# Kernel tuning notes

Measured on AMD Instinct MI355X. Metric: run time of the kernel, lower is better.

The kernel has to match this reference:

```python
import jax, jax.numpy as jnp
import numpy as np

B = 64                      # batch_size
MAX_STEPS = 100
FEAT = 6 + MAX_STEPS        # 106
REPEATS = 10
D = REPEATS * FEAT          # 1060
H = 256                     # policy_hidden_size
COUNTS = 32 * np.arange(B) + 16   # ragged segment sizes, sum=65536, max=2032
N = int(COUNTS.sum())
MAXLEN = int(COUNTS.max())
BN_EPS = 1e-5
LRELU_SLOPE = 0.01


def setup_inputs() -> dict:
    key = jax.random.key(0)
    k = jax.random.split(key, 6)
    seg = np.repeat(np.arange(B), COUNTS).astype(np.float32)  # column 0 = batch index
    features = jax.random.normal(k[0], (N, 1 + FEAT), jnp.float32)
    features = features.at[:, 0].set(jnp.asarray(seg))
    W1 = jax.random.normal(k[1], (D, H), jnp.float32) / np.sqrt(D)
    b1 = jax.random.normal(k[2], (H,), jnp.float32) * 0.01
    W2 = jax.random.normal(k[3], (H, 1), jnp.float32) / np.sqrt(H)
    b2 = jax.random.normal(k[4], (1,), jnp.float32) * 0.01
    return {
        "features": features,
        "bn_gamma": jnp.ones((D,), jnp.float32),
        "bn_beta": jnp.zeros((D,), jnp.float32),
        "W1": W1, "b1": b1, "W2": W2, "b2": b2,
        "max_len": MAXLEN,
    }


def reference(features, bn_gamma, bn_beta, W1, b1, W2, b2, max_len):
    seg = features[:, 0].astype(jnp.int32)                 # [N] batch indices
    x = jnp.tile(features[:, 1:], (1, REPEATS))            # [N, D] repeated features
    # BatchNorm1d (training mode: biased batch stats, as in the torch default)
    mean = jnp.mean(x, axis=0)
    var = jnp.var(x, axis=0)
    xn = (x - mean) * jax.lax.rsqrt(var + BN_EPS) * bn_gamma + bn_beta
    h = jnp.dot(xn, W1) + b1                               # [N, H]
    h = jnp.where(h >= 0, h, LRELU_SLOPE * h)              # LeakyReLU
    logits = (jnp.dot(h, W2) + b2)[:, 0]                   # [N]
    # segmented (ragged) log_softmax over each batch element's nodes
    m = jax.ops.segment_max(logits, seg, num_segments=B)   # [B]
    z = logits - m[seg]
    s = jax.ops.segment_sum(jnp.exp(z), seg, num_segments=B)
    logp = z - jnp.log(s)[seg]                             # [N]
    # scatter into padded [B, max_len] (-inf padding), position = rank within segment
    cnts = jax.ops.segment_sum(jnp.ones_like(seg), seg, num_segments=B)
    starts = jnp.cumsum(cnts) - cnts                       # exclusive prefix sum
    pos = jnp.arange(N, dtype=jnp.int32) - starts[seg]
    out = jnp.full((B, max_len), -jnp.inf, jnp.float32)
    return out.at[seg, pos].set(logp)
```

## Files before the change

kernel.cpp:

```cpp
#include <hip/hip_runtime.h>
#include <math.h>

#define NROWS   65536
#define NFEAT   106
#define NCOLIN  107
#define DREP    10
#define HID     256
#define BATCH   64
#define MAXLEN  2032
#define BN_EPS  1e-5f
#define SLOPE   0.01f
#define KPAD    128
#define NB_STATS 512
#define NEG_BIG (-1.0e30f)

#define WS_PART   0
#define WS_BACC   (WS_PART + NB_STATS*212)
#define WS_W1T    (WS_BACC + HID)
#define WS_FT     (WS_W1T + (HID*KPAD)/2)
#define WS_LOGITS (WS_FT + (NROWS*KPAD)/2)

typedef __attribute__((ext_vector_type(8))) short short8v;
typedef __attribute__((ext_vector_type(4))) float f32x4;

__device__ inline unsigned short f2bf(float x) {
    unsigned int u = __float_as_uint(x);
    return (unsigned short)((u + 0x7FFFu + ((u >> 16) & 1u)) >> 16);
}

__device__ __forceinline__ void gload_lds16(const void* g, void* l) {
    __builtin_amdgcn_global_load_lds(
        (const __attribute__((address_space(1))) void*)(g),
        (__attribute__((address_space(3))) void*)(l), 16, 0, 0);
}

__global__ __launch_bounds__(256) void k_stats(const float* __restrict__ feat,
                                               const float* __restrict__ b1,
                                               float* __restrict__ ws) {
    int tid  = threadIdx.x;
    int wave = tid >> 6, lane = tid & 63;
    int gw   = blockIdx.x * 4 + wave;
    if (blockIdx.x == 0) ws[WS_BACC + tid] = b1[tid];

    unsigned char* ft = (unsigned char*)(ws + WS_FT);
    int c0 = 2 * lane, c1 = 2 * lane + 1;
    bool act = (lane < 53);
    float s0 = 0.f, q0 = 0.f, s1 = 0.f, q1 = 0.f;
    for (int r = gw; r < NROWS; r += 2048) {
        const float* row = feat + (size_t)r * NCOLIN + 1;
        float v0 = 0.f, v1 = 0.f;
        if (act) { v0 = row[c0]; v1 = row[c1]; }
        s0 += v0; q0 += v0 * v0;
        s1 += v1; q1 += v1 * v1;
        unsigned int u = ((unsigned int)f2bf(v1) << 16) | f2bf(v0);
        size_t off = (size_t)(r >> 6) * 16384 + (size_t)((r & 63) * 256 + ((lane * 4) ^ ((r & 7) << 4)));
        *(unsigned int*)(ft + off) = u;
    }
    __shared__ float red[4][64][4];
    red[wave][lane][0] = s0; red[wave][lane][1] = q0;
    red[wave][lane][2] = s1; red[wave][lane][3] = q1;
    __syncthreads();
    if (tid < 53) {
        float S0 = 0.f, Q0 = 0.f, S1 = 0.f, Q1 = 0.f;
        for (int w = 0; w < 4; ++w) {
            S0 += red[w][tid][0]; Q0 += red[w][tid][1];
            S1 += red[w][tid][2]; Q1 += red[w][tid][3];
        }
        float* p = ws + WS_PART + blockIdx.x * 212;
        p[2 * tid] = S0; p[2 * tid + 1] = S1;
        p[106 + 2 * tid] = Q0; p[107 + 2 * tid] = Q1;
    }
}

__global__ __launch_bounds__(256) void k_fold2(const float* __restrict__ gamma,
                                               const float* __restrict__ beta,
                                               const float* __restrict__ W1,
                                               float* __restrict__ ws) {
    int k = blockIdx.x;
    int j = threadIdx.x;
    unsigned char* w1t = (unsigned char*)(ws + WS_W1T);
    int byteW = j * 256 + ((2 * k) ^ ((j & 7) << 4));
    if (k >= NFEAT) { *(unsigned short*)(w1t + byteW) = 0; return; }

    float S = ws[WS_PART + j * 212 + k]       + ws[WS_PART + (j + 256) * 212 + k];
    float Q = ws[WS_PART + j * 212 + 106 + k] + ws[WS_PART + (j + 256) * 212 + 106 + k];
    #pragma unroll
    for (int o = 32; o > 0; o >>= 1) { S += __shfl_xor(S, o); Q += __shfl_xor(Q, o); }
    __shared__ float r8[8];
    int w = j >> 6, l = j & 63;
    if (l == 0) { r8[w * 2] = S; r8[w * 2 + 1] = Q; }
    __syncthreads();
    S = r8[0] + r8[2] + r8[4] + r8[6];
    Q = r8[1] + r8[3] + r8[5] + r8[7];

    float mean = S * (1.0f / NROWS);
    float var  = Q * (1.0f / NROWS) - mean * mean;
    float rstd = rsqrtf(var + BN_EPS);

    float accW = 0.f, accB = 0.f;
    #pragma unroll
    for (int r = 0; r < DREP; ++r) {
        int d = r * NFEAT + k;
        float wv = W1[(size_t)d * HID + j];
        accW += gamma[d] * wv;
        accB += beta[d]  * wv;
    }
    float a = accW * rstd;
    *(unsigned short*)(w1t + byteW) = f2bf(a);
    atomicAdd(&ws[WS_BACC + j], accB - mean * a);
}

__global__ __launch_bounds__(256) void k_mlp2(const float* __restrict__ W2,
                                              const float* __restrict__ b2,
                                              float* __restrict__ ws) {
    __shared__ __align__(16) unsigned char lds[81920];
    unsigned char* wl = lds;
    unsigned char* fl = lds + 65536;

    int tid = threadIdx.x;
    int w = tid >> 6, l = tid & 63;
    int lq = l >> 4, ln = l & 15;

    const unsigned char* wsrc = (const unsigned char*)(ws + WS_W1T);
    #pragma unroll
    for (int i = 0; i < 16; ++i)
        gload_lds16(wsrc + (w * 16 + i) * 1024 + l * 16, wl + (w * 16 + i) * 1024);

    float b1r[16], w2r[16];
    #pragma unroll
    for (int ct = 0; ct < 16; ++ct) {
        b1r[ct] = ws[WS_BACC + ct * 16 + ln];
        w2r[ct] = W2[ct * 16 + ln];
    }
    float bias2 = b2[0];
    __syncthreads();

    const unsigned char* ftb = (const unsigned char*)(ws + WS_FT);
    for (int tile = blockIdx.x; tile < NROWS / 64; tile += gridDim.x) {
        const unsigned char* src = ftb + (size_t)tile * 16384 + w * 4096;
        #pragma unroll
        for (int i = 0; i < 4; ++i)
            gload_lds16(src + i * 1024 + l * 16, fl + w * 4096 + i * 1024);
        asm volatile("s_waitcnt vmcnt(0)" ::: "memory");

        int arow = w * 16 + ln;
        short8v a[4];
        #pragma unroll
        for (int ks = 0; ks < 4; ++ks) {
            int kb = ks * 64 + lq * 16;
            a[ks] = *(const short8v*)(fl + arow * 256 + (kb ^ ((arow & 7) << 4)));
        }
        float sp[4] = {0.f, 0.f, 0.f, 0.f};
        #pragma unroll 4
        for (int ct = 0; ct < 16; ++ct) {
            int j = ct * 16 + ln;
            f32x4 acc = {0.f, 0.f, 0.f, 0.f};
            #pragma unroll
            for (int ks = 0; ks < 4; ++ks) {
                int kb = ks * 64 + lq * 16;
                short8v bfg = *(const short8v*)(wl + j * 256 + (kb ^ ((j & 7) << 4)));
                acc = __builtin_amdgcn_mfma_f32_16x16x32_bf16(a[ks], bfg, acc, 0, 0, 0);
            }
            #pragma unroll
            for (int reg = 0; reg < 4; ++reg) {
                float h = acc[reg] + b1r[ct];
                h = (h >= 0.f) ? h : SLOPE * h;
                sp[reg] += h * w2r[ct];
            }
        }
        #pragma unroll
        for (int reg = 0; reg < 4; ++reg) {
            float s = sp[reg];
            s += __shfl_xor(s, 1); s += __shfl_xor(s, 2);
            s += __shfl_xor(s, 4); s += __shfl_xor(s, 8);
            if (ln == 0)
                ws[WS_LOGITS + tile * 64 + w * 16 + lq * 4 + reg] = s + bias2;
        }
    }
}

__global__ __launch_bounds__(256) void k_softmax(const float* __restrict__ ws,
                                                 float* __restrict__ out) {
    int b = blockIdx.x;
    int tid = threadIdx.x;
    int cnt = 32 * b + 16;
    int start = 16 * b * b;
    __shared__ float cache[MAXLEN];
    __shared__ float red[8];
    const float* lg = ws + WS_LOGITS + start;
    for (int i = tid; i < cnt; i += 256) cache[i] = lg[i];
    __syncthreads();

    float m = -1.0e30f;
    for (int i = tid; i < cnt; i += 256) m = fmaxf(m, cache[i]);
    #pragma unroll
    for (int o = 32; o > 0; o >>= 1) m = fmaxf(m, __shfl_xor(m, o));
    int wave = tid >> 6, lane = tid & 63;
    if (lane == 0) red[wave] = m;
    __syncthreads();
    m = fmaxf(fmaxf(red[0], red[1]), fmaxf(red[2], red[3]));

    float s = 0.f;
    for (int i = tid; i < cnt; i += 256) s += expf(cache[i] - m);
    #pragma unroll
    for (int o = 32; o > 0; o >>= 1) s += __shfl_xor(s, o);
    if (lane == 0) red[4 + wave] = s;
    __syncthreads();
    s = red[4] + red[5] + red[6] + red[7];
    float logC = m + logf(s);

    float* op = out + (size_t)b * MAXLEN;
    for (int i = tid; i < MAXLEN; i += 256)
        op[i] = (i < cnt) ? cache[i] - logC : NEG_BIG;
}

extern "C" void kernel_launch(void* const* d_in, const int* in_sizes, int n_in,
                              void* d_out, int out_size, void* d_ws, size_t ws_size,
                              hipStream_t stream) {
    const float* feat  = (const float*)d_in[0];
    const float* gamma = (const float*)d_in[1];
    const float* beta  = (const float*)d_in[2];
    const float* W1    = (const float*)d_in[3];
    const float* b1    = (const float*)d_in[4];
    const float* W2    = (const float*)d_in[5];
    const float* b2    = (const float*)d_in[6];
    float* ws  = (float*)d_ws;
    float* out = (float*)d_out;

    hipLaunchKernelGGL(k_stats,   dim3(NB_STATS), dim3(256), 0, stream, feat, b1, ws);
    hipLaunchKernelGGL(k_fold2,   dim3(KPAD),     dim3(256), 0, stream, gamma, beta, W1, ws);
    hipLaunchKernelGGL(k_mlp2,    dim3(512),      dim3(256), 0, stream, W2, b2, ws);
    hipLaunchKernelGGL(k_softmax, dim3(BATCH),    dim3(256), 0, stream, ws, out);
}
```

Before: 42.39 us.

## Hold W1 fragments in registers and stream A directly from global

```diff
diff --git a/kernel.cpp b/kernel.cpp
--- a/kernel.cpp
+++ b/kernel.cpp
@@ -28,12 +28,6 @@
     return (unsigned short)((u + 0x7FFFu + ((u >> 16) & 1u)) >> 16);
 }
 
-__device__ __forceinline__ void gload_lds16(const void* g, void* l) {
-    __builtin_amdgcn_global_load_lds(
-        (const __attribute__((address_space(1))) void*)(g),
-        (__attribute__((address_space(3))) void*)(l), 16, 0, 0);
-}
-
 __global__ __launch_bounds__(256) void k_stats(const float* __restrict__ feat,
                                                const float* __restrict__ b1,
                                                float* __restrict__ ws) {
@@ -53,8 +47,7 @@
         s0 += v0; q0 += v0 * v0;
         s1 += v1; q1 += v1 * v1;
         unsigned int u = ((unsigned int)f2bf(v1) << 16) | f2bf(v0);
-        size_t off = (size_t)(r >> 6) * 16384 + (size_t)((r & 63) * 256 + ((lane * 4) ^ ((r & 7) << 4)));
-        *(unsigned int*)(ft + off) = u;
+        *(unsigned int*)(ft + (size_t)r * 256 + lane * 4) = u;
     }
     __shared__ float red[4][64][4];
     red[wave][lane][0] = s0; red[wave][lane][1] = q0;
@@ -79,7 +72,7 @@
     int k = blockIdx.x;
     int j = threadIdx.x;
     unsigned char* w1t = (unsigned char*)(ws + WS_W1T);
-    int byteW = j * 256 + ((2 * k) ^ ((j & 7) << 4));
+    int byteW = j * 256 + 2 * k;
     if (k >= NFEAT) { *(unsigned short*)(w1t + byteW) = 0; return; }
 
     float S = ws[WS_PART + j * 212 + k]       + ws[WS_PART + (j + 256) * 212 + k];
@@ -110,21 +103,23 @@
     atomicAdd(&ws[WS_BACC + j], accB - mean * a);
 }
 
-__global__ __launch_bounds__(256) void k_mlp2(const float* __restrict__ W2,
-                                              const float* __restrict__ b2,
-                                              float* __restrict__ ws) {
-    __shared__ __align__(16) unsigned char lds[81920];
-    unsigned char* wl = lds;
-    unsigned char* fl = lds + 65536;
-
+__global__ __launch_bounds__(256, 1) void k_mlp3(const float* __restrict__ W2,
+                                                 const float* __restrict__ b2,
+                                                 float* __restrict__ ws) {
     int tid = threadIdx.x;
     int w = tid >> 6, l = tid & 63;
     int lq = l >> 4, ln = l & 15;
-
-    const unsigned char* wsrc = (const unsigned char*)(ws + WS_W1T);
-    #pragma unroll
-    for (int i = 0; i < 16; ++i)
-        gload_lds16(wsrc + (w * 16 + i) * 1024 + l * 16, wl + (w * 16 + i) * 1024);
+    int gwid = blockIdx.x * 4 + w;
+
+    const unsigned char* w1t = (const unsigned char*)(ws + WS_W1T);
+    const unsigned char* ftb = (const unsigned char*)(ws + WS_FT);
+
+    short8v bq[16][4];
+    #pragma unroll
+    for (int ct = 0; ct < 16; ++ct)
+        #pragma unroll
+        for (int ks = 0; ks < 4; ++ks)
+            bq[ct][ks] = *(const short8v*)(w1t + (ct * 16 + ln) * 256 + ks * 64 + lq * 16);
 
     float b1r[16], w2r[16];
     #pragma unroll
@@ -133,37 +128,33 @@
         w2r[ct] = W2[ct * 16 + ln];
     }
     float bias2 = b2[0];
-    __syncthreads();
-
-    const unsigned char* ftb = (const unsigned char*)(ws + WS_FT);
-    for (int tile = blockIdx.x; tile < NROWS / 64; tile += gridDim.x) {
-        const unsigned char* src = ftb + (size_t)tile * 16384 + w * 4096;
-        #pragma unroll
-        for (int i = 0; i < 4; ++i)
-            gload_lds16(src + i * 1024 + l * 16, fl + w * 4096 + i * 1024);
-        asm volatile("s_waitcnt vmcnt(0)" ::: "memory");
-
-        int arow = w * 16 + ln;
-        short8v a[4];
-        #pragma unroll
-        for (int ks = 0; ks < 4; ++ks) {
-            int kb = ks * 64 + lq * 16;
-            a[ks] = *(const short8v*)(fl + arow * 256 + (kb ^ ((arow & 7) << 4)));
+
+    const unsigned char* abase = ftb + (size_t)gwid * 64 * 256;
+    int aoff = ln * 256 + lq * 16;
+
+    short8v a0[4], a1[4];
+    #pragma unroll
+    for (int ks = 0; ks < 4; ++ks)
+        a0[ks] = *(const short8v*)(abase + aoff + ks * 64);
+
+    #pragma unroll
+    for (int t = 0; t < 4; ++t) {
+        if (t < 3) {
+            const unsigned char* an = abase + (t + 1) * 4096;
+            #pragma unroll
+            for (int ks = 0; ks < 4; ++ks)
+                a1[ks] = *(const short8v*)(an + aoff + ks * 64);
         }
         float sp[4] = {0.f, 0.f, 0.f, 0.f};
-        #pragma unroll 4
+        #pragma unroll
         for (int ct = 0; ct < 16; ++ct) {
-            int j = ct * 16 + ln;
-            f32x4 acc = {0.f, 0.f, 0.f, 0.f};
+            f32x4 acc = {b1r[ct], b1r[ct], b1r[ct], b1r[ct]};
             #pragma unroll
-            for (int ks = 0; ks < 4; ++ks) {
-                int kb = ks * 64 + lq * 16;
-                short8v bfg = *(const short8v*)(wl + j * 256 + (kb ^ ((j & 7) << 4)));
-                acc = __builtin_amdgcn_mfma_f32_16x16x32_bf16(a[ks], bfg, acc, 0, 0, 0);
-            }
+            for (int ks = 0; ks < 4; ++ks)
+                acc = __builtin_amdgcn_mfma_f32_16x16x32_bf16(a0[ks], bq[ct][ks], acc, 0, 0, 0);
             #pragma unroll
             for (int reg = 0; reg < 4; ++reg) {
-                float h = acc[reg] + b1r[ct];
+                float h = acc[reg];
                 h = (h >= 0.f) ? h : SLOPE * h;
                 sp[reg] += h * w2r[ct];
             }
@@ -174,8 +165,10 @@
             s += __shfl_xor(s, 1); s += __shfl_xor(s, 2);
             s += __shfl_xor(s, 4); s += __shfl_xor(s, 8);
             if (ln == 0)
-                ws[WS_LOGITS + tile * 64 + w * 16 + lq * 4 + reg] = s + bias2;
-        }
+                ws[WS_LOGITS + gwid * 64 + t * 16 + lq * 4 + reg] = s + bias2;
+        }
+        #pragma unroll
+        for (int ks = 0; ks < 4; ++ks) a0[ks] = a1[ks];
     }
 }
 
@@ -229,6 +222,6 @@
 
     hipLaunchKernelGGL(k_stats,   dim3(NB_STATS), dim3(256), 0, stream, feat, b1, ws);
     hipLaunchKernelGGL(k_fold2,   dim3(KPAD),     dim3(256), 0, stream, gamma, beta, W1, ws);
-    hipLaunchKernelGGL(k_mlp2,    dim3(512),      dim3(256), 0, stream, W2, b2, ws);
+    hipLaunchKernelGGL(k_mlp3,    dim3(256),      dim3(256), 0, stream, W2, b2, ws);
     hipLaunchKernelGGL(k_softmax, dim3(BATCH),    dim3(256), 0, stream, ws, out);
 }
```

Measured after the change: 47.43 us. +11.9%, slower.
